# Kernel optimization log

Measured on AMD Instinct MI355X. Metric: run time of the kernel, lower is better.

The kernel has to match this reference:

```python
import jax, jax.numpy as jnp
import numpy as np

B, T, DIM = 2, 2048, 2048
H, HKV = 16, 4
D = DIM // H          # head_dim = 128
G = H // HKV          # GQA group = 4
ROPE_BASE = 10000.0
TRAIN_SEQ_LEN = 1024  # Rotary default; T > this triggers NTK base rescale


def _rope_tables():
    # Faithful to Rotary.forward: NTK scaling when seq_len > train_seq_len.
    if T > TRAIN_SEQ_LEN:
        sc = T / TRAIN_SEQ_LEN
        base = ROPE_BASE * sc ** (D / (D - 2))
    else:
        base = ROPE_BASE
    inv = 1.0 / base ** (np.arange(0, D, 2, dtype=np.float32) / D)  # [D/2]
    f = np.outer(np.arange(T, dtype=np.float32), inv)               # [T, D/2]
    cos = jnp.asarray(np.cos(f), jnp.float32)[None, :, None, :]     # [1,T,1,D/2]
    sin = jnp.asarray(np.sin(f), jnp.float32)[None, :, None, :]
    return cos, sin


def _rms_norm(x):
    # F.rms_norm with no weight: x / sqrt(mean(x^2) + eps), eps = finfo(dtype).eps
    eps = jnp.finfo(x.dtype).eps
    return x * jax.lax.rsqrt(jnp.mean(x * x, axis=-1, keepdims=True) + eps)


def _apply_rope(x, cos, sin):
    x1, x2 = jnp.split(x, 2, axis=-1)
    return jnp.concatenate([x1 * cos + x2 * sin, -x1 * sin + x2 * cos], axis=-1)


def setup_inputs() -> dict:
    key = jax.random.key(0)
    kx, kq, kk, kv, kp = jax.random.split(key, 5)
    s = lambda fan_in: 1.0 / np.sqrt(fan_in)
    kv_dim = HKV * D
    return {
        "x": jax.random.normal(kx, (B, T, DIM), jnp.float32),
        "Wq": jax.random.normal(kq, (DIM, DIM), jnp.float32) * s(DIM),
        "Wk": jax.random.normal(kk, (kv_dim, DIM), jnp.float32) * s(DIM),
        "Wv": jax.random.normal(kv, (kv_dim, DIM), jnp.float32) * s(DIM),
        "Wproj": jax.random.normal(kp, (DIM, DIM), jnp.float32) * s(DIM),
        "q_gain": jnp.full((H,), 1.0, jnp.float32),
    }


def reference(x, Wq, Wk, Wv, Wproj, q_gain):
    # QKV projections (bias-free linears)
    q = (x @ Wq.T).reshape(B, T, H, D)
    k = (x @ Wk.T).reshape(B, T, HKV, D)
    v = (x @ Wv.T).reshape(B, T, HKV, D)

    # QK RMSNorm + RoPE + per-head q gain
    q = _rms_norm(q)
    k = _rms_norm(k)
    cos, sin = _rope_tables()
    q = _apply_rope(q, cos, sin)
    k = _apply_rope(k, cos, sin)
    q = q * q_gain[None, None, :, None]

    # GQA causal SDPA without materializing repeated K/V:
    # group query heads by kv head: q -> [B,T,HKV,G,D]
    qg = q.reshape(B, T, HKV, G, D)
    scores = jnp.einsum('btkgd,bskd->bkgts', qg, k) / np.sqrt(D)  # [B,HKV,G,T,T]
    causal = jnp.tril(jnp.ones((T, T), bool))
    scores = jnp.where(causal[None, None, None], scores, -jnp.inf)
    p = jax.nn.softmax(scores, axis=-1)
    y = jnp.einsum('bkgts,bskd->btkgd', p, v).reshape(B, T, H, D)

    out = y.reshape(B, T, DIM) @ Wproj.T
    return out, v
```

## Files before the change

### kernel.cpp

```cpp
#include <hip/hip_runtime.h>
#include <hip/hip_bf16.h>

typedef __bf16 bf16_t;
typedef __bf16 bf16x4 __attribute__((ext_vector_type(4)));
typedef __bf16 bf16x8 __attribute__((ext_vector_type(8)));
typedef float f32x4 __attribute__((ext_vector_type(4)));

#define B_    2
#define T_    2048
#define DIM_  2048
#define H_    16
#define HKV_  4
#define D_    128
#define KVDIM_ 512

__device__ __forceinline__ bf16x8 cvt8(f32x4 a, f32x4 b) {
  bf16x8 r;
  r[0] = (bf16_t)a[0]; r[1] = (bf16_t)a[1]; r[2] = (bf16_t)a[2]; r[3] = (bf16_t)a[3];
  r[4] = (bf16_t)b[0]; r[5] = (bf16_t)b[1]; r[6] = (bf16_t)b[2]; r[7] = (bf16_t)b[3];
  return r;
}
__device__ __forceinline__ bf16x4 cvt4(f32x4 a) {
  bf16x4 r;
  r[0] = (bf16_t)a[0]; r[1] = (bf16_t)a[1]; r[2] = (bf16_t)a[2]; r[3] = (bf16_t)a[3];
  return r;
}
__device__ __forceinline__ void g2l16(const void* g, void* l) {
  __builtin_amdgcn_global_load_lds(
      (const __attribute__((address_space(1))) unsigned int*)g,
      (__attribute__((address_space(3))) unsigned int*)l, 16, 0, 0);
}

__global__ __launch_bounds__(256)
void cvt_all(const float* __restrict__ x,  const float* __restrict__ wq,
             const float* __restrict__ wk, const float* __restrict__ wv,
             const float* __restrict__ wp, bf16_t* __restrict__ xb,
             bf16_t* __restrict__ wqkvb, bf16_t* __restrict__ wpb) {
  int blk = blockIdx.x;
  const float* s; bf16_t* d; int lb;
  if (blk < 4096)      { s = x;  d = xb;                              lb = blk; }
  else if (blk < 6144) { s = wq; d = wqkvb;                           lb = blk - 4096; }
  else if (blk < 6656) { s = wk; d = wqkvb + (size_t)2048 * DIM_;     lb = blk - 6144; }
  else if (blk < 7168) { s = wv; d = wqkvb + (size_t)2560 * DIM_;     lb = blk - 6656; }
  else                 { s = wp; d = wpb;                             lb = blk - 7168; }
  size_t i = (size_t)lb * 2048 + (size_t)threadIdx.x * 8;
  f32x4 a = *(const f32x4*)(s + i);
  f32x4 b = *(const f32x4*)(s + i + 4);
  *(bf16x8*)(d + i) = cvt8(a, b);
}

template <int MODE, bool AASYNC, bool WASYNC>
__global__ __launch_bounds__(256)
void gemm128(const void* __restrict__ Ag, const void* __restrict__ Wg,
             const void* __restrict__ Wg2, void* __restrict__ Cb,
             bf16_t* __restrict__ Kb, bf16_t* __restrict__ Vb,
             float* __restrict__ Vf, int M, int N, int K) {
  constexpr int LDA = AASYNC ? 32 : 40;
  constexpr int LDW = WASYNC ? 32 : 40;
  __shared__ bf16_t As[128 * LDA];
  __shared__ bf16_t Ws[128 * LDW];
  const int tid  = threadIdx.x;
  const int wave = tid >> 6, lane = tid & 63;
  const int l16  = lane & 15, lg = lane >> 4;
  const int m0 = blockIdx.y * 128, n0 = blockIdx.x * 128;
  const int wm = (wave & 1) * 64, wn = (wave >> 1) * 64;
  f32x4 acc[4][4] = {};

  for (int k0 = 0; k0 < K; k0 += 32) {
    __syncthreads();
    if constexpr (AASYNC) {
      const bf16_t* A = (const bf16_t*)Ag;
      const int r = lane >> 2, c8 = (lane & 3) * 8;
      g2l16(&A[(size_t)(m0 + wave * 32 + r) * K + k0 + c8],      &As[(wave * 32) * LDA]);
      g2l16(&A[(size_t)(m0 + wave * 32 + 16 + r) * K + k0 + c8], &As[(wave * 32 + 16) * LDA]);
    } else {
      const float* A = (const float*)Ag;
#pragma unroll
      for (int j = 0; j < 4; j++) {
        int row = wave * 32 + j * 8 + (lane >> 3);
        int cf  = (lane & 7) * 4;
        f32x4 v = *(const f32x4*)&A[(size_t)(m0 + row) * K + k0 + cf];
        *(bf16x4*)&As[row * LDA + cf] = cvt4(v);
      }
    }
    if constexpr (WASYNC) {
      const bf16_t* W = (const bf16_t*)Wg;
      const int r = lane >> 2, c8 = (lane & 3) * 8;
      g2l16(&W[(size_t)(n0 + wave * 32 + r) * K + k0 + c8],      &Ws[(wave * 32) * LDW]);
      g2l16(&W[(size_t)(n0 + wave * 32 + 16 + r) * K + k0 + c8], &Ws[(wave * 32 + 16) * LDW]);
    } else {
      const float* W;
      int nb;
      if constexpr (MODE == 3) {
        if (n0 < 512) { W = (const float*)Wg;  nb = n0; }
        else          { W = (const float*)Wg2; nb = n0 - 512; }
      } else { W = (const float*)Wg; nb = n0; }
#pragma unroll
      for (int j = 0; j < 4; j++) {
        int row = wave * 32 + j * 8 + (lane >> 3);
        int cf  = (lane & 7) * 4;
        f32x4 v = *(const f32x4*)&W[(size_t)(nb + row) * K + k0 + cf];
        *(bf16x4*)&Ws[row * LDW + cf] = cvt4(v);
      }
    }
    __syncthreads();
    bf16x8 af[4], bfr[4];
#pragma unroll
    for (int i = 0; i < 4; i++)
      af[i] = *(const bf16x8*)&As[(wm + i * 16 + l16) * LDA + lg * 8];
#pragma unroll
    for (int j = 0; j < 4; j++)
      bfr[j] = *(const bf16x8*)&Ws[(wn + j * 16 + l16) * LDW + lg * 8];
#pragma unroll
    for (int i = 0; i < 4; i++)
#pragma unroll
      for (int j = 0; j < 4; j++)
        acc[i][j] = __builtin_amdgcn_mfma_f32_16x16x32_bf16(af[i], bfr[j], acc[i][j], 0, 0, 0);
  }
#pragma unroll
  for (int i = 0; i < 4; i++)
#pragma unroll
    for (int j = 0; j < 4; j++) {
      int row = m0 + wm + i * 16 + lg * 4;
      int col = n0 + wn + j * 16 + l16;
#pragma unroll
      for (int r = 0; r < 4; r++) {
        float v = acc[i][j][r];
        if constexpr (MODE == 0) {
          ((bf16_t*)Cb)[(size_t)(row + r) * N + col] = (bf16_t)v;
        } else if constexpr (MODE == 2) {
          ((float*)Cb)[(size_t)(row + r) * N + col] = v;
        } else if constexpr (MODE == 1) {
          if (col < 2048)      ((bf16_t*)Cb)[(size_t)(row + r) * 2048 + col] = (bf16_t)v;
          else if (col < 2560) Kb[(size_t)(row + r) * 512 + (col - 2048)] = (bf16_t)v;
          else {
            int c = col - 2560;
            Vb[(size_t)(row + r) * 512 + c] = (bf16_t)v;
            Vf[(size_t)(row + r) * 512 + c] = v;
          }
        } else {
          if (col < 512) ((bf16_t*)Cb)[(size_t)(row + r) * 512 + col] = (bf16_t)v;
          else {
            int c = col - 512;
            Vb[(size_t)(row + r) * 512 + c] = (bf16_t)v;
            Vf[(size_t)(row + r) * 512 + c] = v;
          }
        }
      }
    }
}

#define SB() __builtin_amdgcn_sched_barrier(0)
#define BARRIER() __builtin_amdgcn_s_barrier()
#define LGKM0() do { asm volatile("s_waitcnt lgkmcnt(0)" ::: "memory"); SB(); } while (0)
#define VMW(N) do { asm volatile("s_waitcnt vmcnt(" #N ")" ::: "memory"); SB(); } while (0)

#define RD_A(BUF, QM) do { \
  _Pragma("unroll") for (int f_ = 0; f_ < 4; f_++) { \
    const int r_ = wm * 128 + (QM) * 64 + f_ * 16 + l16; \
    _Pragma("unroll") for (int ks_ = 0; ks_ < 2; ks_++) \
      a[f_][ks_] = *(const bf16x8*)(lds + (BUF) * 65536 + r_ * 128 + ((ks_ * 64 + lg * 16) ^ swz)); \
  } } while (0)

#define RD_B(BUF, QN, BB) do { \
  _Pragma("unroll") for (int n_ = 0; n_ < 2; n_++) { \
    const int r_ = wn * 64 + (QN) * 32 + n_ * 16 + l16; \
    _Pragma("unroll") for (int ks_ = 0; ks_ < 2; ks_++) \
      BB[n_][ks_] = *(const bf16x8*)(lds + (BUF) * 65536 + 32768 + r_ * 128 + ((ks_ * 64 + lg * 16) ^ swz)); \
  } } while (0)

#define MM(QM, QN, BB) do { \
  __builtin_amdgcn_s_setprio(1); \
  _Pragma("unroll") for (int f_ = 0; f_ < 4; f_++) \
    _Pragma("unroll") for (int n_ = 0; n_ < 2; n_++) \
      _Pragma("unroll") for (int ks_ = 0; ks_ < 2; ks_++) \
        acc[(QM) * 4 + f_][(QN) * 2 + n_] = __builtin_amdgcn_mfma_f32_16x16x32_bf16( \
            a[f_][ks_], BB[n_][ks_], acc[(QM) * 4 + f_][(QN) * 2 + n_], 0, 0, 0); \
  __builtin_amdgcn_s_setprio(0); \
  } while (0)

#define K_ITER(KT0, LAST) do { \
  const int kA1_ = ((KT0) + 1) * 64; \
  const int kN2_ = ((KT0) + 2) * 64; \
  const int kN3_ = ((KT0) + 3) * 64; \
   \
  RD_A(0, 0); RD_B(0, 0, b0); \
  stage_half(Ag, m0, kA1_, 65536); \
  asm volatile("s_waitcnt lgkmcnt(8)" ::: "memory"); \
  SB(); BARRIER(); LGKM0(); \
  MM(0, 0, b0); \
  SB(); BARRIER(); \
   \
  RD_B(0, 1, b1); \
  stage_half(Ag, m0 + 128, kA1_, 65536 + 16384); \
  SB(); BARRIER(); LGKM0(); \
  MM(0, 1, b1); \
  SB(); BARRIER(); \
   \
  RD_A(0, 1); \
  if (!(LAST)) stage_half(Wg, n0, kN2_, 32768); \
  SB(); BARRIER(); LGKM0(); \
  MM(1, 0, b0); \
  SB(); BARRIER(); \
   \
  if (!(LAST)) { stage_half(Wg, n0 + 128, kN2_, 32768 + 16384); VMW(4); } \
  else { VMW(0); } \
  SB(); BARRIER(); \
  MM(1, 1, b1); \
  SB(); BARRIER(); \
   \
  RD_A(1, 0); RD_B(1, 0, b0); \
  if (!(LAST)) stage_half(Ag, m0, kN2_, 0); \
  asm volatile("s_waitcnt lgkmcnt(8)" ::: "memory"); \
  SB(); BARRIER(); LGKM0(); \
  MM(0, 0, b0); \
  SB(); BARRIER(); \
   \
  RD_B(1, 1, b1); \
  if (!(LAST)) stage_half(Ag, m0 + 128, kN2_, 16384); \
  SB(); BARRIER(); LGKM0(); \
  MM(0, 1, b1); \
  SB(); BARRIER(); \
   \
  RD_A(1, 1); \
  if (!(LAST)) stage_half(Wg, n0, kN3_, 65536 + 32768); \
  SB(); BARRIER(); LGKM0(); \
  MM(1, 0, b0); \
  SB(); BARRIER(); \
   \
  if (!(LAST)) { stage_half(Wg, n0 + 128, kN3_, 65536 + 32768 + 16384); VMW(4); } \
  SB(); BARRIER(); \
  MM(1, 1, b1); \
  SB(); BARRIER(); \
} while (0)

template <int MODE>
__global__ __launch_bounds__(512, 2)
void gemm256(const bf16_t* __restrict__ Ag, const bf16_t* __restrict__ Wg,
             void* __restrict__ Cb, bf16_t* __restrict__ Kb, bf16_t* __restrict__ Vb,
             float* __restrict__ Vf, int M, int N, int K) {
  (void)M;
  __shared__ __align__(16) char lds[131072];
  const int tid  = threadIdx.x;
  const int wave = tid >> 6, lane = tid & 63;
  const int l16  = lane & 15, lg = lane >> 4;
  const int wm = wave >> 2, wn = wave & 3;
  const int swz = (l16 & 7) << 4;
  const int m0 = blockIdx.y * 256, n0 = blockIdx.x * 256;
  const int srow = lane >> 3;
  const int scol = ((lane & 7) ^ srow) * 8;

  auto stage_half = [&](const bf16_t* __restrict__ X, int xrow, int k0, int ldsoff) {
    const bf16_t* src = X + (size_t)(xrow + wave * 16 + srow) * K + (k0 + scol);
    char* dst = lds + ldsoff + wave * 2048;
    g2l16(src, dst);
    g2l16(src + (size_t)8 * K, dst + 1024);
  };

  f32x4 acc[8][4] = {};
  bf16x8 a[4][2], b0[2][2], b1[2][2];

  stage_half(Ag, m0,        0, 0);
  stage_half(Ag, m0 + 128,  0, 16384);
  stage_half(Wg, n0,        0, 32768);
  stage_half(Wg, n0 + 128,  0, 32768 + 16384);
  stage_half(Wg, n0,       64, 65536 + 32768);
  stage_half(Wg, n0 + 128, 64, 65536 + 32768 + 16384);
  VMW(4);
  BARRIER();

  const int NIT = K >> 7;
  for (int it = 0; it < NIT - 1; ++it) {
    K_ITER(2 * it, 0);
  }
  K_ITER(2 * (NIT - 1), 1);

#pragma unroll
  for (int mf = 0; mf < 8; mf++)
#pragma unroll
    for (int nf = 0; nf < 4; nf++) {
      const int row = m0 + wm * 128 + mf * 16 + lg * 4;
      const int col = n0 + wn * 64 + nf * 16 + l16;
#pragma unroll
      for (int r = 0; r < 4; r++) {
        float v = acc[mf][nf][r];
        if constexpr (MODE == 1) {
          if (col < 2048)      ((bf16_t*)Cb)[(size_t)(row + r) * 2048 + col] = (bf16_t)v;
          else if (col < 2560) Kb[(size_t)(row + r) * 512 + (col - 2048)] = (bf16_t)v;
          else {
            int c = col - 2560;
            Vb[(size_t)(row + r) * 512 + c] = (bf16_t)v;
            Vf[(size_t)(row + r) * 512 + c] = v;
          }
        } else {
          ((float*)Cb)[(size_t)(row + r) * N + col] = v;
        }
      }
    }
}

__global__ __launch_bounds__(256)
void qk_norm_rope(bf16_t* __restrict__ Qp, bf16_t* __restrict__ Kp,
                  const float* __restrict__ gain) {
  const int lane = threadIdx.x & 63;
  int row = blockIdx.x * 4 + (threadIdx.x >> 6);
  bf16_t* Xp; int nh; bool ag;
  const int MQ = B_ * T_ * H_;
  if (row < MQ) { Xp = Qp; nh = H_;  ag = true; }
  else          { Xp = Kp; nh = HKV_; ag = false; row -= MQ; }
  const int h = row % nh;
  const int t = (row / nh) % T_;
  bf16_t* p = Xp + (size_t)row * D_;
  float x0 = (float)p[lane * 2 + 0];
  float x1 = (float)p[lane * 2 + 1];
  float ss = x0 * x0 + x1 * x1;
#pragma unroll
  for (int m = 32; m >= 1; m >>= 1) ss += __shfl_xor(ss, m);
  const float rn = rsqrtf(ss * (1.0f / 128.0f) + 1.1920929e-07f);
  x0 *= rn; x1 *= rn;
  const float y0 = __shfl_xor(x0, 32);
  const float y1 = __shfl_xor(x1, 32);
  const int i0 = (lane & 31) * 2;
  const float kfreq = -0.22349352180347601f;
  float s0, c0, s1, c1;
  float a0 = (float)t * exp2f(kfreq * (float)i0);
  float a1 = (float)t * exp2f(kfreq * (float)(i0 + 1));
  sincosf(a0, &s0, &c0);
  sincosf(a1, &s1, &c1);
  float o0, o1;
  if (lane < 32) { o0 = x0 * c0 + y0 * s0;  o1 = x1 * c1 + y1 * s1; }
  else           { o0 = x0 * c0 - y0 * s0;  o1 = x1 * c1 - y1 * s1; }
  if (ag) { float g = gain[h]; o0 *= g; o1 *= g; }
  p[lane * 2 + 0] = (bf16_t)o0;
  p[lane * 2 + 1] = (bf16_t)o1;
}

#define VLD 72

__global__ __launch_bounds__(256, 2)
void flash_attn(const bf16_t* __restrict__ Q, const bf16_t* __restrict__ Kg,
                const bf16_t* __restrict__ V, bf16_t* __restrict__ Y) {
  __shared__ bf16_t Ks[2][64 * 128];
  __shared__ bf16_t Vs[2][D_ * VLD];
  const int tid  = threadIdx.x;
  const int wave = tid >> 6, lane = tid & 63;
  const int l16  = lane & 15, lg = lane >> 4;
  const int b = blockIdx.z, h = blockIdx.y;
  const int pi = blockIdx.x;
  const int hk = h >> 2;

  int qr[2];
  qr[0] = 64 * pi + 16 * wave;
  qr[1] = 64 * (31 - pi) + 16 * wave;

  bf16x8 qf[2][4];
#pragma unroll
  for (int mt = 0; mt < 2; mt++)
#pragma unroll
    for (int kk = 0; kk < 4; kk++)
      qf[mt][kk] = *(const bf16x8*)&Q[(((size_t)b * T_ + qr[mt] + l16) * H_ + h) * D_ + kk * 32 + lg * 8];

  f32x4 o[2][8] = {};
  float lsum[2] = {};
  const float C = 0.12752531f;

  const int sp2 = (tid & 31) * 2;
  const int dvh = (tid >> 5) * 8;
  const int ssl = (sp2 & 3) | (((sp2 >> 4) & 1) << 2) | (((sp2 >> 2) & 1) << 3)
                | (((sp2 >> 3) & 1) << 4) | (sp2 & 32);

  bf16x8 vreg[2][2];
  auto vload = [&](int k0) {
#pragma unroll
    for (int it = 0; it < 2; it++) {
      const bf16_t* vb = &V[(((size_t)b * T_ + k0 + sp2) * HKV_ + hk) * D_ + dvh + it * 64];
      vreg[it][0] = *(const bf16x8*)vb;
      vreg[it][1] = *(const bf16x8*)(vb + HKV_ * D_);
    }
  };
  auto vstore = [&](int buf) {
#pragma unroll
    for (int it = 0; it < 2; it++) {
      int dd = dvh + it * 64;
      const unsigned short* au = (const unsigned short*)&vreg[it][0];
      const unsigned short* bu = (const unsigned short*)&vreg[it][1];
#pragma unroll
      for (int i = 0; i < 8; i++) {
        unsigned int pr = (unsigned int)au[i] | ((unsigned int)bu[i] << 16);
        *(unsigned int*)&Vs[buf][(dd + i) * VLD + ssl] = pr;
      }
    }
  };
  auto kstage = [&](int buf, int k0) {
#pragma unroll
    for (int j = 0; j < 4; j++) {
      const int rbase = wave * 16 + j * 4;
      const int row = rbase + (lane >> 4);
      const int cf = ((lane & 15) ^ (row & 7)) * 8;
      g2l16(&Kg[(((size_t)b * T_ + k0 + row) * HKV_ + hk) * D_ + cf],
            (char*)&Ks[buf][0] + rbase * 256);
    }
  };

  const int nkb = 32 - pi;
  kstage(0, 0);
  vload(0);
  VMW(0);
  vstore(0);
  LGKM0();
  BARRIER();

  for (int kb = 0; kb < nkb; kb++) {
    const int k0 = kb * 64;
    const int cur = kb & 1, nxt = cur ^ 1;
    const bool more = (kb + 1 < nkb);
    if (more) { kstage(nxt, k0 + 64); vload(k0 + 64); }

    const bool act0 = (kb <= pi);

    f32x4 s[2][4] = {};
#pragma unroll
    for (int kk = 0; kk < 4; kk++) {
      bf16x8 kf[4];
#pragma unroll
      for (int f = 0; f < 4; f++)
        kf[f] = *(const bf16x8*)((const char*)&Ks[cur][0] + (f * 16 + l16) * 256
                                 + ((kk * 64 + lg * 16) ^ ((l16 & 7) << 4)));
      __builtin_amdgcn_s_setprio(1);
      if (act0)
#pragma unroll
        for (int f = 0; f < 4; f++)
          s[0][f] = __builtin_amdgcn_mfma_f32_16x16x32_bf16(kf[f], qf[0][kk], s[0][f], 0, 0, 0);
#pragma unroll
      for (int f = 0; f < 4; f++)
        s[1][f] = __builtin_amdgcn_mfma_f32_16x16x32_bf16(kf[f], qf[1][kk], s[1][f], 0, 0, 0);
      __builtin_amdgcn_s_setprio(0);
    }
    bf16x8 pfr[2][2];
#pragma unroll
    for (int mt = 0; mt < 2; mt++) {
      if (mt == 0 && !act0) continue;
      const bool diag = (mt == 0) ? (kb == pi) : (kb == nkb - 1);
      const int myq = qr[mt] + l16;
      if (diag) {
#pragma unroll
        for (int f = 0; f < 4; f++)
#pragma unroll
          for (int r = 0; r < 4; r++) {
            int kg = k0 + f * 16 + lg * 4 + r;
            float p = (kg <= myq) ? exp2f(s[mt][f][r] * C) : 0.0f;
            lsum[mt] += p;
            s[mt][f][r] = p;
          }
      } else {
#pragma unroll
        for (int f = 0; f < 4; f++)
#pragma unroll
          for (int r = 0; r < 4; r++) {
            float p = exp2f(s[mt][f][r] * C);
            lsum[mt] += p;
            s[mt][f][r] = p;
          }
      }
      pfr[mt][0] = cvt8(s[mt][0], s[mt][1]);
      pfr[mt][1] = cvt8(s[mt][2], s[mt][3]);
    }
    if (more) vstore(nxt);
#pragma unroll
    for (int f = 0; f < 8; f++) {
      bf16x8 v0 = *(const bf16x8*)&Vs[cur][(f * 16 + l16) * VLD + lg * 8];
      bf16x8 v1 = *(const bf16x8*)&Vs[cur][(f * 16 + l16) * VLD + 32 + lg * 8];
      __builtin_amdgcn_s_setprio(1);
      if (act0) {
        o[0][f] = __builtin_amdgcn_mfma_f32_16x16x32_bf16(pfr[0][0], v0, o[0][f], 0, 0, 0);
        o[0][f] = __builtin_amdgcn_mfma_f32_16x16x32_bf16(pfr[0][1], v1, o[0][f], 0, 0, 0);
      }
      o[1][f] = __builtin_amdgcn_mfma_f32_16x16x32_bf16(pfr[1][0], v0, o[1][f], 0, 0, 0);
      o[1][f] = __builtin_amdgcn_mfma_f32_16x16x32_bf16(pfr[1][1], v1, o[1][f], 0, 0, 0);
      __builtin_amdgcn_s_setprio(0);
    }
    if (more) {
      VMW(0);
      LGKM0();
      BARRIER();
    }
  }
#pragma unroll
  for (int mt = 0; mt < 2; mt++) {
    float l = lsum[mt];
    l += __shfl_xor(l, 16);
    l += __shfl_xor(l, 32);
    const float inv = 1.0f / l;
    float rlv[4];
#pragma unroll
    for (int r = 0; r < 4; r++) rlv[r] = __shfl(inv, lg * 4 + r);
#pragma unroll
    for (int f = 0; f < 8; f++)
#pragma unroll
      for (int r = 0; r < 4; r++) {
        int t = qr[mt] + lg * 4 + r;
        Y[(((size_t)b * T_ + t) * H_ + h) * D_ + f * 16 + l16] = (bf16_t)(o[mt][f][r] * rlv[r]);
      }
  }
}

extern "C" void kernel_launch(void* const* d_in, const int* in_sizes, int n_in,
                              void* d_out, int out_size, void* d_ws, size_t ws_size,
                              hipStream_t stream) {
  (void)in_sizes; (void)n_in; (void)out_size;
  const float* x     = (const float*)d_in[0];
  const float* Wq    = (const float*)d_in[1];
  const float* Wk    = (const float*)d_in[2];
  const float* Wv    = (const float*)d_in[3];
  const float* Wproj = (const float*)d_in[4];
  const float* qgain = (const float*)d_in[5];

  float* out  = (float*)d_out;
  float* vout = out + (size_t)B_ * T_ * DIM_;

  const size_t M = (size_t)B_ * T_;
  char* ws = (char*)d_ws;
  size_t off = 0;
  auto take = [&](size_t elems) { bf16_t* p = (bf16_t*)(ws + off); off += elems * sizeof(bf16_t); return p; };

  bf16_t* Qp = take(M * DIM_);
  bf16_t* Kp = take(M * KVDIM_);
  bf16_t* Vb = take(M * KVDIM_);

  const size_t cvt_elems = M * DIM_ + (size_t)3072 * DIM_ + (size_t)DIM_ * DIM_;
  const bool fast = (ws_size >= off + cvt_elems * sizeof(bf16_t));

  dim3 blk(256);
  if (fast) {
    bf16_t* xb     = take(M * DIM_);
    bf16_t* Wqkvb  = take((size_t)3072 * DIM_);
    bf16_t* Wpb    = take((size_t)DIM_ * DIM_);

    cvt_all<<<dim3(9216), blk, 0, stream>>>(x, Wq, Wk, Wv, Wproj, xb, Wqkvb, Wpb);

    gemm256<1><<<dim3(3072 / 256, M / 256), dim3(512), 0, stream>>>(
        xb, Wqkvb, Qp, Kp, Vb, vout, (int)M, 3072, DIM_);

    qk_norm_rope<<<dim3((unsigned)((M * H_ + M * HKV_) / 4)), blk, 0, stream>>>(Qp, Kp, qgain);
    flash_attn<<<dim3(16, H_, B_), blk, 0, stream>>>(Qp, Kp, Vb, Qp);

    gemm256<2><<<dim3(DIM_ / 256, M / 256), dim3(512), 0, stream>>>(
        Qp, Wpb, out, nullptr, nullptr, nullptr, (int)M, DIM_, DIM_);
  } else {
    gemm128<0, false, false><<<dim3(DIM_ / 128, M / 128), blk, 0, stream>>>(
        x, Wq, nullptr, Qp, nullptr, nullptr, nullptr, M, DIM_, DIM_);
    gemm128<3, false, false><<<dim3(2 * KVDIM_ / 128, M / 128), blk, 0, stream>>>(
        x, Wk, Wv, Kp, nullptr, Vb, vout, M, 2 * KVDIM_, DIM_);
    qk_norm_rope<<<dim3((unsigned)((M * H_ + M * HKV_) / 4)), blk, 0, stream>>>(Qp, Kp, qgain);
    flash_attn<<<dim3(16, H_, B_), blk, 0, stream>>>(Qp, Kp, Vb, Qp);
    gemm128<2, true, false><<<dim3(DIM_ / 128, M / 128), blk, 0, stream>>>(
        Qp, Wproj, nullptr, out, nullptr, nullptr, nullptr, M, DIM_, DIM_);
  }
}
```

Before: 323.2 us.

## Single-buffer V tile in LDS with 4-row packed transpose stores

Each thread now loads four consecutive V rows and writes 8-byte packed transposed pairs into the LDS tile, instead of two rows with 4-byte stores. The V tile drops from double to single buffering, which cuts LDS footprint. The transposed store moves to the top of each iteration between two __syncthreads, and the explicit wait/barrier at the loop end is removed. Risks: an extra barrier per iteration, and the V store latency is no longer hidden behind the QK compute.

```diff
diff --git a/kernel.cpp b/kernel.cpp
--- a/kernel.cpp
+++ b/kernel.cpp
@@ -5,6 +5,7 @@
 typedef __bf16 bf16x4 __attribute__((ext_vector_type(4)));
 typedef __bf16 bf16x8 __attribute__((ext_vector_type(8)));
 typedef float f32x4 __attribute__((ext_vector_type(4)));
+typedef unsigned int uint2_t __attribute__((ext_vector_type(2)));
 
 #define B_    2
 #define T_    2048
@@ -341,7 +342,7 @@
 void flash_attn(const bf16_t* __restrict__ Q, const bf16_t* __restrict__ Kg,
                 const bf16_t* __restrict__ V, bf16_t* __restrict__ Y) {
   __shared__ bf16_t Ks[2][64 * 128];
-  __shared__ bf16_t Vs[2][D_ * VLD];
+  __shared__ bf16_t Vs[D_ * VLD];
   const int tid  = threadIdx.x;
   const int wave = tid >> 6, lane = tid & 63;
   const int l16  = lane & 15, lg = lane >> 4;
@@ -364,31 +365,28 @@
   float lsum[2] = {};
   const float C = 0.12752531f;
 
-  const int sp2 = (tid & 31) * 2;
-  const int dvh = (tid >> 5) * 8;
-  const int ssl = (sp2 & 3) | (((sp2 >> 4) & 1) << 2) | (((sp2 >> 2) & 1) << 3)
-                | (((sp2 >> 3) & 1) << 4) | (sp2 & 32);
-
-  bf16x8 vreg[2][2];
+  const int kb4 = (tid & 15) * 4;
+  const int dch = (tid >> 4) * 8;
+  const int slot4 = (((kb4 >> 4) & 1) << 2) | (((kb4 >> 2) & 1) << 3)
+                  | (((kb4 >> 3) & 1) << 4) | (kb4 & 32);
+
+  bf16x8 vreg4[4];
   auto vload = [&](int k0) {
 #pragma unroll
-    for (int it = 0; it < 2; it++) {
-      const bf16_t* vb = &V[(((size_t)b * T_ + k0 + sp2) * HKV_ + hk) * D_ + dvh + it * 64];
-      vreg[it][0] = *(const bf16x8*)vb;
-      vreg[it][1] = *(const bf16x8*)(vb + HKV_ * D_);
-    }
+    for (int kk = 0; kk < 4; kk++)
+      vreg4[kk] = *(const bf16x8*)&V[(((size_t)b * T_ + k0 + kb4 + kk) * HKV_ + hk) * D_ + dch];
   };
-  auto vstore = [&](int buf) {
-#pragma unroll
-    for (int it = 0; it < 2; it++) {
-      int dd = dvh + it * 64;
-      const unsigned short* au = (const unsigned short*)&vreg[it][0];
-      const unsigned short* bu = (const unsigned short*)&vreg[it][1];
-#pragma unroll
-      for (int i = 0; i < 8; i++) {
-        unsigned int pr = (unsigned int)au[i] | ((unsigned int)bu[i] << 16);
-        *(unsigned int*)&Vs[buf][(dd + i) * VLD + ssl] = pr;
-      }
+  auto vstore = [&]() {
+    const unsigned short* u0 = (const unsigned short*)&vreg4[0];
+    const unsigned short* u1 = (const unsigned short*)&vreg4[1];
+    const unsigned short* u2 = (const unsigned short*)&vreg4[2];
+    const unsigned short* u3 = (const unsigned short*)&vreg4[3];
+#pragma unroll
+    for (int i = 0; i < 8; i++) {
+      uint2_t pr;
+      pr[0] = (unsigned int)u0[i] | ((unsigned int)u1[i] << 16);
+      pr[1] = (unsigned int)u2[i] | ((unsigned int)u3[i] << 16);
+      *(uint2_t*)&Vs[(dch + i) * VLD + slot4] = pr;
     }
   };
   auto kstage = [&](int buf, int k0) {
@@ -405,16 +403,16 @@
   const int nkb = 32 - pi;
   kstage(0, 0);
   vload(0);
-  VMW(0);
-  vstore(0);
-  LGKM0();
-  BARRIER();
 
   for (int kb = 0; kb < nkb; kb++) {
     const int k0 = kb * 64;
-    const int cur = kb & 1, nxt = cur ^ 1;
+    const int cur = kb & 1;
     const bool more = (kb + 1 < nkb);
-    if (more) { kstage(nxt, k0 + 64); vload(k0 + 64); }
+
+    __syncthreads();
+    vstore();
+    __syncthreads();
+    if (more) { kstage(cur ^ 1, k0 + 64); vload(k0 + 64); }
 
     const bool act0 = (kb <= pi);
 
@@ -465,11 +463,10 @@
       pfr[mt][0] = cvt8(s[mt][0], s[mt][1]);
       pfr[mt][1] = cvt8(s[mt][2], s[mt][3]);
     }
-    if (more) vstore(nxt);
 #pragma unroll
     for (int f = 0; f < 8; f++) {
-      bf16x8 v0 = *(const bf16x8*)&Vs[cur][(f * 16 + l16) * VLD + lg * 8];
-      bf16x8 v1 = *(const bf16x8*)&Vs[cur][(f * 16 + l16) * VLD + 32 + lg * 8];
+      bf16x8 v0 = *(const bf16x8*)&Vs[(f * 16 + l16) * VLD + lg * 8];
+      bf16x8 v1 = *(const bf16x8*)&Vs[(f * 16 + l16) * VLD + 32 + lg * 8];
       __builtin_amdgcn_s_setprio(1);
       if (act0) {
         o[0][f] = __builtin_amdgcn_mfma_f32_16x16x32_bf16(pfr[0][0], v0, o[0][f], 0, 0, 0);
@@ -478,11 +475,6 @@
       o[1][f] = __builtin_amdgcn_mfma_f32_16x16x32_bf16(pfr[1][0], v0, o[1][f], 0, 0, 0);
       o[1][f] = __builtin_amdgcn_mfma_f32_16x16x32_bf16(pfr[1][1], v1, o[1][f], 0, 0, 0);
       __builtin_amdgcn_s_setprio(0);
-    }
-    if (more) {
-      VMW(0);
-      LGKM0();
-      BARRIER();
     }
   }
 #pragma unroll
```

New measurement: 322.3 us. Within noise of the previous version (-0.3%).
